# Kernel tuning notes

Measured on AMD Instinct MI355X. Metric: run time of the kernel, lower is better.

## Reference

```python
import jax, jax.numpy as jnp
import numpy as np


def setup_inputs() -> dict:
    key = jax.random.key(0)
    k1, k2, k3 = jax.random.split(key, 3)
    B, N, E, A = 1024, 64, 64, 32
    emb_inputs = jax.random.normal(k1, (B, N, E), dtype=jnp.float32)
    W1 = jax.random.normal(k2, (E, A), dtype=jnp.float32) * (1.0 / np.sqrt(E))
    b1 = jnp.zeros((A,), dtype=jnp.float32)
    W2 = jax.random.normal(k3, (A, 1), dtype=jnp.float32) * (1.0 / np.sqrt(A))
    b2 = jnp.zeros((1,), dtype=jnp.float32)
    return {"emb_inputs": emb_inputs, "W1": W1, "b1": b1, "W2": W2, "b2": b2,
            "num_fields": N}


def reference(emb_inputs, W1, b1, W2, b2, num_fields):
    # Pairwise interaction indices (i < j), same order as torch double loop
    rowidx, colidx = np.triu_indices(num_fields, k=1)
    rowidx = jnp.asarray(rowidx)
    colidx = jnp.asarray(colidx)
    # inner: (B, NC2, E) elementwise product of field pairs
    inner = emb_inputs[:, rowidx] * emb_inputs[:, colidx]
    # tiny attention MLP: E -> A -> 1, softmax over the pair dim
    h = jax.nn.relu(jnp.einsum('bpe,ea->bpa', inner, W1) + b1)
    logits = jnp.einsum('bpa,ao->bpo', h, W2) + b2          # (B, NC2, 1)
    attn_scores = jax.nn.softmax(logits, axis=1)            # (B, NC2, 1)
    # dropout layers are identity in eval mode
    outputs = jnp.sum(inner * attn_scores, axis=1)          # (B, E)
    return outputs, attn_scores
```

## Files before the change

kernel.cpp:

```cpp
#include <hip/hip_runtime.h>

#define BATCH   1024
#define NF      64
#define EDIM    64
#define ADIM    32
#define NPAIR   2016
#define XSTR    72
#define ASTR    68

typedef _Float16 f16;
typedef f16   f16x2  __attribute__((ext_vector_type(2)));
typedef f16   f16x4  __attribute__((ext_vector_type(4)));
typedef f16   f16x8  __attribute__((ext_vector_type(8)));
typedef float f32x2  __attribute__((ext_vector_type(2)));
typedef float f32x4  __attribute__((ext_vector_type(4)));
typedef float f32x16 __attribute__((ext_vector_type(16)));

__device__ __forceinline__ f16x8 asH(int4 v) {
    union { int4 i; f16x8 h; } u; u.i = v; return u.h;
}
__device__ __forceinline__ f16x2 pkrtz(float a, float b) {
    union { __fp16 __attribute__((ext_vector_type(2))) r; f16x2 h; } u;
    u.r = __builtin_amdgcn_cvt_pkrtz(a, b);
    return u.h;
}

__global__ __launch_bounds__(256, 4) void afm_kernel(
    const float* __restrict__ emb,
    const float* __restrict__ W1,
    const float* __restrict__ b1,
    const float* __restrict__ W2,
    const float* __restrict__ b2,
    float* __restrict__ out_vec,
    float* __restrict__ out_attn)
{
    __shared__ __align__(16) f16 xs[NF * XSTR];
    __shared__ __align__(16) f16 Xt[EDIM * XSTR];
    __shared__ __align__(16) f16 As[NF * ASTR];
    __shared__ __align__(16) char Ubuf[NPAIR * 2];
    f16* eh = (f16*)Ubuf;
    float (*partial)[EDIM] = (float (*)[EDIM])Ubuf;
    __shared__ float red[8];

    const int t    = threadIdx.x;
    const int b    = blockIdx.x;
    const int wid  = t >> 6;
    const int lane = t & 63;
    const int g    = lane >> 4;
    const int m16  = lane & 15;
    const int h    = lane >> 5;
    const int l32  = lane & 31;
    const int l16  = lane & 15;
    const int hb   = l32 >> 4;

    const float4* xg4 = (const float4*)(emb + (size_t)b * NF * EDIM);
    #pragma unroll
    for (int it = 0; it < 4; ++it) {
        int idx = t + it * 256;
        int f = idx >> 4, e4 = (idx & 15) * 4;
        float4 v = xg4[idx];
        f16x2 p0 = pkrtz(v.x, v.y);
        f16x2 p1 = pkrtz(v.z, v.w);
        f16x4 pk = {p0.x, p0.y, p1.x, p1.y};
        *(f16x4*)&xs[f * XSTR + e4] = pk;
    }

    f16x8 w1a[4];
    #pragma unroll
    for (int q = 0; q < 4; ++q)
        #pragma unroll
        for (int jj = 0; jj < 8; jj += 2) {
            float fa = W1[(16 * q + 8 * h + jj)     * ADIM + l32];
            float fb = W1[(16 * q + 8 * h + jj + 1) * ADIM + l32];
            f16x2 pk = pkrtz(fa, fb);
            w1a[q][jj] = pk.x; w1a[q][jj + 1] = pk.y;
        }

    f32x2 b1f2[8], w2f2[8];
    #pragma unroll
    for (int rr = 0; rr < 8; ++rr) {
        int r = 2 * rr;
        int a = (r & 3) + 8 * (r >> 2) + 4 * h;
        b1f2[rr] = (f32x2){b1[a], b1[a + 1]};
        w2f2[rr] = (f32x2){W2[a], W2[a + 1]};
    }
    const float b2s = b2[0];
    __syncthreads();

    {
        const unsigned short* xsu = (const unsigned short*)xs;
        #pragma unroll
        for (int it = 0; it < 2; ++it) {
            int cid = t + it * 256;
            int e = cid & 63, c = cid >> 6;
            unsigned int d[4];
            #pragma unroll
            for (int r2 = 0; r2 < 4; ++r2) {
                unsigned lo = xsu[(8 * c + 2 * r2)     * XSTR + e];
                unsigned hi = xsu[(8 * c + 2 * r2 + 1) * XSTR + e];
                d[r2] = lo | (hi << 16);
            }
            int4 w4 = {(int)d[0], (int)d[1], (int)d[2], (int)d[3]};
            *(int4*)&Xt[e * XSTR + 8 * c] = w4;
        }
    }
    __syncthreads();

    int probe = __builtin_amdgcn_mov_dpp(l16, 0x124, 0xF, 0xF, false);
    const bool plus4 = (probe == ((l16 + 4) & 15));
    const int  s0r   = plus4 ? (wid + 1) : (wid + 5);

    int4 xi4[4], xj4[4];

    auto LOADX = [&](int row, int4* d) {
        #pragma unroll
        for (int q = 0; q < 4; ++q)
            d[q] = *(const int4*)&xs[row * XSTR + 16 * q + 8 * h];
    };
    auto ROT4D = [&](int4* d, int& jv) {
        #pragma unroll
        for (int q = 0; q < 4; ++q) {
            d[q].x = __builtin_amdgcn_mov_dpp(d[q].x, 0x124, 0xF, 0xF, false);
            d[q].y = __builtin_amdgcn_mov_dpp(d[q].y, 0x124, 0xF, 0xF, false);
            d[q].z = __builtin_amdgcn_mov_dpp(d[q].z, 0x124, 0xF, 0xF, false);
            d[q].w = __builtin_amdgcn_mov_dpp(d[q].w, 0x124, 0xF, 0xF, false);
        }
        jv = __builtin_amdgcn_mov_dpp(jv, 0x124, 0xF, 0xF, false);
    };
    auto SUB = [&](const int4* xa, const int4* xb, int iv, int jv) {
        f32x16 acc = {};
        #pragma unroll
        for (int q = 0; q < 4; ++q) {
            f16x8 prod = asH(xa[q]) * asH(xb[q]);
            acc = __builtin_amdgcn_mfma_f32_32x32x16_f16(w1a[q], prod, acc, 0, 0, 0);
        }
        f32x2 tr2 = {0.f, 0.f};
        #pragma unroll
        for (int rr = 0; rr < 8; ++rr) {
            f32x2 a2 = {acc[2 * rr], acc[2 * rr + 1]};
            f32x2 h2 = __builtin_elementwise_max(a2 + b1f2[rr], (f32x2){0.f, 0.f});
            tr2 += h2 * w2f2[rr];
        }
        float tr = tr2.x + tr2.y;
        tr += __shfl_xor(tr, 32);
        float ev = __expf(tr + b2s);
        int imin = min(iv, jv), jmax = max(iv, jv);
        int p = ((imin * (127 - imin)) >> 1) + jmax - imin - 1;
        if (lane < 32) {
            f16 ah = (f16)ev;
            eh[p] = ah;
            As[imin * ASTR + jmax] = ah;
            As[jmax * ASTR + imin] = ah;
        }
    };

    LOADX(l32, xi4);
    {
        int jv = 32 + 16 * hb + ((l16 + wid) & 15);
        LOADX(jv, xj4);
        #pragma unroll
        for (int k = 0; k < 4; ++k) {
            SUB(xi4, xj4, l32, jv);
            if (k < 3) ROT4D(xj4, jv);
        }
    }
    {
        int jv = 32 + 16 * (1 - hb) + ((l16 + wid) & 15);
        LOADX(jv, xj4);
        #pragma unroll
        for (int k = 0; k < 4; ++k) {
            SUB(xi4, xj4, l32, jv);
            if (k < 3) ROT4D(xj4, jv);
        }
    }
    {
        int jv = 16 * hb + ((l16 + s0r) & 15);
        LOADX(jv, xj4);
        SUB(xi4, xj4, l32, jv);
        ROT4D(xj4, jv);
        SUB(xi4, xj4, l32, jv);
    }
    {
        int jv = 16 + ((l16 + wid + 8 * hb) & 15);
        LOADX(l16, xi4);
        LOADX(jv, xj4);
        SUB(xi4, xj4, l16, jv);
        ROT4D(xj4, jv);
        SUB(xi4, xj4, l16, jv);
    }
    {
        int jv = 32 + 16 * hb + ((l16 + s0r) & 15);
        LOADX(32 + l32, xi4);
        LOADX(jv, xj4);
        SUB(xi4, xj4, 32 + l32, jv);
        ROT4D(xj4, jv);
        SUB(xi4, xj4, 32 + l32, jv);
    }
    {
        int jv = 48 + ((l16 + wid + 8 * hb) & 15);
        LOADX(32 + l16, xi4);
        LOADX(jv, xj4);
        SUB(xi4, xj4, 32 + l16, jv);
        ROT4D(xj4, jv);
        SUB(xi4, xj4, 32 + l16, jv);
    }
    if (t < NF) As[t * ASTR + t] = (f16)0.f;
    __syncthreads();

    float lv[8];
    #pragma unroll
    for (int k = 0; k < 8; ++k) {
        int p = t + 256 * k;
        lv[k] = (p < NPAIR) ? (float)eh[p] : 0.f;
    }
    float sw = 0.f;
    #pragma unroll
    for (int k = 0; k < 8; ++k) sw += lv[k];
    #pragma unroll
    for (int off = 32; off; off >>= 1) sw += __shfl_xor(sw, off);
    if (lane == 0) red[wid] = sw;
    __syncthreads();
    const float inv = 1.0f / (red[0] + red[1] + red[2] + red[3]);

    #pragma unroll
    for (int k = 0; k < 8; ++k) {
        int p = t + 256 * k;
        if (p < NPAIR) out_attn[(size_t)b * NPAIR + p] = lv[k] * inv;
    }

    const int itile = wid;
    const f16* arow = &As[(itile * 16 + m16) * ASTR];
    f16x4 afa0 = *(const f16x4*)(arow + 8 * g);
    f16x4 afb0 = *(const f16x4*)(arow + 8 * g + 4);
    f16x4 afa1 = *(const f16x4*)(arow + 32 + 8 * g);
    f16x4 afb1 = *(const f16x4*)(arow + 32 + 8 * g + 4);
    f16x8 af0, af1;
    #pragma unroll
    for (int j = 0; j < 4; ++j) {
        af0[j] = afa0[j]; af0[4 + j] = afb0[j];
        af1[j] = afa1[j]; af1[4 + j] = afb1[j];
    }

    f32x4 yacc[4];
    #pragma unroll
    for (int et = 0; et < 4; ++et) yacc[et] = (f32x4){0.f, 0.f, 0.f, 0.f};
    #pragma unroll
    for (int et = 0; et < 4; ++et) {
        const f16* xtr = &Xt[(et * 16 + m16) * XSTR];
        f16x8 bf0 = *(const f16x8*)(xtr + 8 * g);
        f16x8 bf1 = *(const f16x8*)(xtr + 32 + 8 * g);
        yacc[et] = __builtin_amdgcn_mfma_f32_16x16x32_f16(af0, bf0, yacc[et], 0, 0, 0);
        yacc[et] = __builtin_amdgcn_mfma_f32_16x16x32_f16(af1, bf1, yacc[et], 0, 0, 0);
    }

    #pragma unroll
    for (int et = 0; et < 4; ++et) {
        float v = 0.f;
        #pragma unroll
        for (int r = 0; r < 4; ++r) {
            int i = itile * 16 + 4 * g + r;
            int e = et * 16 + m16;
            v = fmaf((float)xs[i * XSTR + e], yacc[et][r], v);
        }
        v += __shfl_xor(v, 16);
        v += __shfl_xor(v, 32);
        if (g == 0) partial[wid][et * 16 + m16] = v;
    }
    __syncthreads();
    if (t < EDIM)
        out_vec[(size_t)b * EDIM + t] = 0.5f * inv *
            (partial[0][t] + partial[1][t] + partial[2][t] + partial[3][t]);
}

extern "C" void kernel_launch(void* const* d_in, const int* in_sizes, int n_in,
                              void* d_out, int out_size, void* d_ws, size_t ws_size,
                              hipStream_t stream) {
    const float* emb = (const float*)d_in[0];
    const float* W1  = (const float*)d_in[1];
    const float* b1  = (const float*)d_in[2];
    const float* W2  = (const float*)d_in[3];
    const float* b2  = (const float*)d_in[4];
    float* out_vec  = (float*)d_out;
    float* out_attn = (float*)d_out + (size_t)BATCH * EDIM;

    afm_kernel<<<BATCH, 256, 0, stream>>>(emb, W1, b1, W2, b2, out_vec, out_attn);
}
```

Baseline: 24.12 us.

## Split MFMA chain, fold bias into accumulator, replace DPP rotations with LDS loads

The pair-scoring inner loop now runs two independent MFMA accumulator chains and sums them, so MFMA dependency latency can overlap. The b1 bias is preloaded into the first accumulator instead of being added afterwards. b2 is dropped because softmax is shift-invariant. The DPP lane-rotation scheme and its runtime probe are replaced by direct LDS loads of each j row, and one barrier after the transpose is removed. This trades cross-lane moves for more LDS traffic and adds register pressure from the second accumulator.

```diff
diff --git a/kernel.cpp b/kernel.cpp
--- a/kernel.cpp
+++ b/kernel.cpp
@@ -76,15 +76,15 @@
             w1a[q][jj] = pk.x; w1a[q][jj + 1] = pk.y;
         }
 
-    f32x2 b1f2[8], w2f2[8];
+    f32x16 b1acc;
+    #pragma unroll
+    for (int r = 0; r < 16; ++r) b1acc[r] = b1[(r & 3) + 8 * (r >> 2) + 4 * h];
+    f32x2 w2f2[8];
     #pragma unroll
     for (int rr = 0; rr < 8; ++rr) {
-        int r = 2 * rr;
-        int a = (r & 3) + 8 * (r >> 2) + 4 * h;
-        b1f2[rr] = (f32x2){b1[a], b1[a + 1]};
+        int a = ((2 * rr) & 3) + 8 * ((2 * rr) >> 2) + 4 * h;
         w2f2[rr] = (f32x2){W2[a], W2[a + 1]};
     }
-    const float b2s = b2[0];
     __syncthreads();
 
     {
@@ -104,12 +104,8 @@
             *(int4*)&Xt[e * XSTR + 8 * c] = w4;
         }
     }
-    __syncthreads();
-
-    int probe = __builtin_amdgcn_mov_dpp(l16, 0x124, 0xF, 0xF, false);
-    const bool plus4 = (probe == ((l16 + 4) & 15));
-    const int  s0r   = plus4 ? (wid + 1) : (wid + 5);
-
+
+    const f32x16 zacc = {};
     int4 xi4[4], xj4[4];
 
     auto LOADX = [&](int row, int4* d) {
@@ -117,33 +113,26 @@
         for (int q = 0; q < 4; ++q)
             d[q] = *(const int4*)&xs[row * XSTR + 16 * q + 8 * h];
     };
-    auto ROT4D = [&](int4* d, int& jv) {
-        #pragma unroll
-        for (int q = 0; q < 4; ++q) {
-            d[q].x = __builtin_amdgcn_mov_dpp(d[q].x, 0x124, 0xF, 0xF, false);
-            d[q].y = __builtin_amdgcn_mov_dpp(d[q].y, 0x124, 0xF, 0xF, false);
-            d[q].z = __builtin_amdgcn_mov_dpp(d[q].z, 0x124, 0xF, 0xF, false);
-            d[q].w = __builtin_amdgcn_mov_dpp(d[q].w, 0x124, 0xF, 0xF, false);
-        }
-        jv = __builtin_amdgcn_mov_dpp(jv, 0x124, 0xF, 0xF, false);
-    };
-    auto SUB = [&](const int4* xa, const int4* xb, int iv, int jv) {
-        f32x16 acc = {};
-        #pragma unroll
-        for (int q = 0; q < 4; ++q) {
-            f16x8 prod = asH(xa[q]) * asH(xb[q]);
-            acc = __builtin_amdgcn_mfma_f32_32x32x16_f16(w1a[q], prod, acc, 0, 0, 0);
-        }
+    auto SUBX = [&](const int4* xa, const int4* xb, int iv, int jv) {
+        f16x8 p0 = asH(xa[0]) * asH(xb[0]);
+        f16x8 p1 = asH(xa[1]) * asH(xb[1]);
+        f16x8 p2 = asH(xa[2]) * asH(xb[2]);
+        f16x8 p3 = asH(xa[3]) * asH(xb[3]);
+        f32x16 accA = __builtin_amdgcn_mfma_f32_32x32x16_f16(w1a[0], p0, b1acc, 0, 0, 0);
+        f32x16 accB = __builtin_amdgcn_mfma_f32_32x32x16_f16(w1a[2], p2, zacc, 0, 0, 0);
+        accA = __builtin_amdgcn_mfma_f32_32x32x16_f16(w1a[1], p1, accA, 0, 0, 0);
+        accB = __builtin_amdgcn_mfma_f32_32x32x16_f16(w1a[3], p3, accB, 0, 0, 0);
         f32x2 tr2 = {0.f, 0.f};
         #pragma unroll
         for (int rr = 0; rr < 8; ++rr) {
-            f32x2 a2 = {acc[2 * rr], acc[2 * rr + 1]};
-            f32x2 h2 = __builtin_elementwise_max(a2 + b1f2[rr], (f32x2){0.f, 0.f});
+            f32x2 a2 = {accA[2 * rr] + accB[2 * rr],
+                        accA[2 * rr + 1] + accB[2 * rr + 1]};
+            f32x2 h2 = __builtin_elementwise_max(a2, (f32x2){0.f, 0.f});
             tr2 += h2 * w2f2[rr];
         }
         float tr = tr2.x + tr2.y;
         tr += __shfl_xor(tr, 32);
-        float ev = __expf(tr + b2s);
+        float ev = __expf(tr);
         int imin = min(iv, jv), jmax = max(iv, jv);
         int p = ((imin * (127 - imin)) >> 1) + jmax - imin - 1;
         if (lane < 32) {
@@ -155,54 +144,44 @@
     };
 
     LOADX(l32, xi4);
-    {
-        int jv = 32 + 16 * hb + ((l16 + wid) & 15);
-        LOADX(jv, xj4);
-        #pragma unroll
-        for (int k = 0; k < 4; ++k) {
-            SUB(xi4, xj4, l32, jv);
-            if (k < 3) ROT4D(xj4, jv);
-        }
-    }
-    {
-        int jv = 32 + 16 * (1 - hb) + ((l16 + wid) & 15);
-        LOADX(jv, xj4);
-        #pragma unroll
-        for (int k = 0; k < 4; ++k) {
-            SUB(xi4, xj4, l32, jv);
-            if (k < 3) ROT4D(xj4, jv);
-        }
-    }
-    {
-        int jv = 16 * hb + ((l16 + s0r) & 15);
-        LOADX(jv, xj4);
-        SUB(xi4, xj4, l32, jv);
-        ROT4D(xj4, jv);
-        SUB(xi4, xj4, l32, jv);
-    }
-    {
-        int jv = 16 + ((l16 + wid + 8 * hb) & 15);
-        LOADX(l16, xi4);
-        LOADX(jv, xj4);
-        SUB(xi4, xj4, l16, jv);
-        ROT4D(xj4, jv);
-        SUB(xi4, xj4, l16, jv);
-    }
-    {
-        int jv = 32 + 16 * hb + ((l16 + s0r) & 15);
-        LOADX(32 + l32, xi4);
-        LOADX(jv, xj4);
-        SUB(xi4, xj4, 32 + l32, jv);
-        ROT4D(xj4, jv);
-        SUB(xi4, xj4, 32 + l32, jv);
-    }
-    {
-        int jv = 48 + ((l16 + wid + 8 * hb) & 15);
-        LOADX(32 + l16, xi4);
-        LOADX(jv, xj4);
-        SUB(xi4, xj4, 32 + l16, jv);
-        ROT4D(xj4, jv);
-        SUB(xi4, xj4, 32 + l16, jv);
+    #pragma unroll
+    for (int k = 0; k < 4; ++k) {
+        int jv = 32 + 16 * hb + ((l16 + wid + 4 * k) & 15);
+        LOADX(jv, xj4);
+        SUBX(xi4, xj4, l32, jv);
+    }
+    #pragma unroll
+    for (int k = 0; k < 4; ++k) {
+        int jv = 32 + 16 * (1 - hb) + ((l16 + wid + 4 * k) & 15);
+        LOADX(jv, xj4);
+        SUBX(xi4, xj4, l32, jv);
+    }
+    #pragma unroll
+    for (int k = 0; k < 2; ++k) {
+        int jv = 16 * hb + ((l16 + wid + 1 + 4 * k) & 15);
+        LOADX(jv, xj4);
+        SUBX(xi4, xj4, l32, jv);
+    }
+    LOADX(l16, xi4);
+    #pragma unroll
+    for (int k = 0; k < 2; ++k) {
+        int jv = 16 + ((l16 + wid + 8 * hb + 4 * k) & 15);
+        LOADX(jv, xj4);
+        SUBX(xi4, xj4, l16, jv);
+    }
+    LOADX(32 + l32, xi4);
+    #pragma unroll
+    for (int k = 0; k < 2; ++k) {
+        int jv = 32 + 16 * hb + ((l16 + wid + 1 + 4 * k) & 15);
+        LOADX(jv, xj4);
+        SUBX(xi4, xj4, 32 + l32, jv);
+    }
+    LOADX(32 + l16, xi4);
+    #pragma unroll
+    for (int k = 0; k < 2; ++k) {
+        int jv = 48 + ((l16 + wid + 8 * hb + 4 * k) & 15);
+        LOADX(jv, xj4);
+        SUBX(xi4, xj4, 32 + l16, jv);
     }
     if (t < NF) As[t * ASTR + t] = (f16)0.f;
     __syncthreads();
@@ -280,6 +259,7 @@
     const float* b1  = (const float*)d_in[2];
     const float* W2  = (const float*)d_in[3];
     const float* b2  = (const float*)d_in[4];
+    (void)b2;
     float* out_vec  = (float*)d_out;
     float* out_attn = (float*)d_out + (size_t)BATCH * EDIM;
 
```

Measured after the change: 23.84 us. No clear change (-1.2%).
